# Performance work log

Measured on AMD Instinct MI355X. Metric: run time of the kernel, lower is better.

## Reference

```python
import jax, jax.numpy as jnp
import numpy as np

B, T, C, L = 1024, 1024, 96, 32
BLANK = C - 1          # tf.compat.v1.nn.ctc_loss uses num_classes-1 as blank
S = 2 * L + 1          # extended label length (blanks interleaved)
NEG = -1e30            # log-space 'zero'


def setup_inputs() -> dict:
    key = jax.random.key(0)
    k1, k2 = jax.random.split(key)
    y_true = jax.random.randint(k1, (B, L), 0, BLANK).astype(jnp.int64)  # labels in [0, C-2]
    y_pred = jax.random.normal(k2, (B, T, C), dtype=jnp.float32)          # pre-softmax logits
    return {"y_true": y_true, "y_pred": y_pred}


def _ctc_loss(y_pred, y_true):
    # y_pred: [B,T,C] logits, y_true: [B,L] int labels. All lengths are full
    # (label_length = L, input_length = T), matching the layer's call().
    logp = jax.nn.log_softmax(y_pred, axis=-1)                   # [B,T,C]
    # extended labels: blank, l0, blank, l1, ..., blank  -> [B,S]
    ext = jnp.full((B, S), BLANK, dtype=jnp.int32).at[:, 1::2].set(y_true.astype(jnp.int32))
    # skip transition allowed where ext[s] != blank and ext[s] != ext[s-2]
    skip = jnp.concatenate(
        [jnp.zeros((B, 2), bool), (ext[:, 2:] != BLANK) & (ext[:, 2:] != ext[:, :-2])],
        axis=1)                                                  # [B,S]
    # per-time emission log-probs of extended labels: [T,B,S]
    lp_ext = jnp.take_along_axis(logp, ext[:, None, :], axis=2)  # [B,T,S]
    lp_ext = jnp.transpose(lp_ext, (1, 0, 2))                    # [T,B,S]

    alpha0 = (jnp.full((B, S), NEG, dtype=logp.dtype)
              .at[:, 0].set(lp_ext[0, :, 0])
              .at[:, 1].set(lp_ext[0, :, 1]))

    def step(alpha, lp_t):
        a_stay = alpha
        a_prev = jnp.concatenate([jnp.full((B, 1), NEG, alpha.dtype), alpha[:, :-1]], axis=1)
        a_skip = jnp.concatenate([jnp.full((B, 2), NEG, alpha.dtype), alpha[:, :-2]], axis=1)
        a_skip = jnp.where(skip, a_skip, NEG)
        m = jnp.maximum(jnp.maximum(a_stay, a_prev), a_skip)
        new = m + jnp.log(jnp.exp(a_stay - m) + jnp.exp(a_prev - m) + jnp.exp(a_skip - m))
        return new + lp_t, None

    alphaT, _ = jax.lax.scan(step, alpha0, lp_ext[1:])
    # total log-likelihood ends at last blank or last label
    end = jnp.stack([alphaT[:, S - 1], alphaT[:, S - 2]], axis=0)  # [2,B]
    loss = -jax.scipy.special.logsumexp(end, axis=0)               # [B]
    return loss[:, None]                                           # [B,1], as ctc_batch_cost


def reference(y_true, y_pred):
    return _ctc_loss(y_pred, y_true)
```

## Files before the change

kernel.cpp:

```cpp
#include <hip/hip_runtime.h>


#define NB 1024
#define NT 1024
#define NC 96
#define NL 32
#define NEGF (-1e30f)
#define CHUNK 32
#define NCHUNK (NT / CHUNK)
#define SLOTF 97
#define LOG2E 1.4426950408889634f
#define LN2   0.69314718055994531f

__device__ __forceinline__ float fexp2(float x) { return __builtin_amdgcn_exp2f(x); }
__device__ __forceinline__ float flog2(float x) { return __builtin_amdgcn_logf(x); }

template <int CTRL>
__device__ __forceinline__ float dpp_mov(float v) {
  return __int_as_float(__builtin_amdgcn_update_dpp(
      __float_as_int(v), __float_as_int(v), CTRL, 0xF, 0xF, false));
}
__device__ __forceinline__ float dpp_shr1(float oldv, float v) {
  return __int_as_float(__builtin_amdgcn_update_dpp(
      __float_as_int(oldv), __float_as_int(v), 0x138, 0xF, 0xF, false));
}

__global__ __launch_bounds__(256) void ctc_fused(const int* __restrict__ yt,
                                                 const float* __restrict__ yp,
                                                 float* __restrict__ out) {
  __shared__ float ring[2 * CHUNK * SLOTF];

  const int b = blockIdx.x;
  const int wid = threadIdx.x >> 6;
  const int lane = threadIdx.x & 63;

  const float* __restrict__ xrow = yp + (size_t)b * NT * NC;

  const int cw = b & 3;
  const bool is_cons = (wid == cw);
  const int pr = ((wid - cw + 4) & 3) - 1;

  int extc = 95;
  bool skipf = false;
  if (is_cons) {
    const int* lab = yt + b * NL;
    if ((lane & 1) == 0) {
      const int j = lane >> 1;
      extc = lab[j];
      skipf = (j > 0) && (extc != lab[j - 1]);
    }
    __builtin_amdgcn_s_setprio(1);
  }

  const int rsel = lane >> 5;
  const int l32 = lane & 31;

  float UA[6][3], UB[6][3];

  auto load_regs = [&](float (&U)[6][3], int t0) {
    const float* rp = xrow + (size_t)(t0 + 2 * pr + rsel) * NC + l32;
#pragma unroll
    for (int jj = 0; jj < 6; ++jj) {
      if (pr + 3 * jj < 16) {
        U[jj][0] = rp[jj * 6 * NC + 0];
        U[jj][1] = rp[jj * 6 * NC + 32];
        U[jj][2] = rp[jj * 6 * NC + 64];
      }
    }
  };

  auto compute_store = [&](float (&U)[6][3], int cc) {
    float* wb = ring + (cc & 1) * (CHUNK * SLOTF) + (2 * pr + rsel) * SLOTF + l32;
#pragma unroll
    for (int jj = 0; jj < 6; ++jj) {
      if (pr + 3 * jj < 16) {
        const float u0 = U[jj][0] * LOG2E;
        const float u1 = U[jj][1] * LOG2E;
        const float u2 = U[jj][2] * LOG2E;
        float z = fexp2(u0) + fexp2(u1) + fexp2(u2);
        z += dpp_mov<0xB1>(z);
        z += dpp_mov<0x4E>(z);
        z += dpp_mov<0x124>(z);
        z += dpp_mov<0x128>(z);
        z += __shfl_xor(z, 16);
        const float lz = flog2(z);
        wb[jj * 6 * SLOTF + 0]  = u0 - lz;
        wb[jj * 6 * SLOTF + 32] = u1 - lz;
        wb[jj * 6 * SLOTF + 64] = u2 - lz;
      }
    }
  };

  float alpha = NEGF;
  float a0 = NEGF;

  auto consume = [&](int cc, bool first) {
    const float* hb = ring + (cc & 1) * (CHUNK * SLOTF) + extc;
    const float* hb95 = ring + (cc & 1) * (CHUNK * SLOTF) + 95;
    float lq[4], lqb[4];
    lq[0] = hb[0 * SLOTF];  lqb[0] = hb95[0 * SLOTF];
    lq[1] = hb[1 * SLOTF];  lqb[1] = hb95[1 * SLOTF];
    lq[2] = hb[2 * SLOTF];  lqb[2] = hb95[2 * SLOTF];
    lq[3] = 0.0f;           lqb[3] = 0.0f;
#pragma unroll
    for (int tt = 0; tt < CHUNK; ++tt) {
      const float lp = lq[tt & 3];
      const float lpb = lqb[tt & 3];
      if (tt + 3 < CHUNK) {
        lq[(tt + 3) & 3] = hb[(tt + 3) * SLOTF];
        lqb[(tt + 3) & 3] = hb95[(tt + 3) * SLOTF];
      }
      if (first && tt == 0) {
        a0 = lpb;
        alpha = (lane == 0) ? lp : NEGF;
      } else {
        const float ap = dpp_shr1(a0, alpha);
        float as = dpp_shr1(NEGF, ap);
        as = skipf ? as : NEGF;
        float mm, mid, mn;
        asm("v_max3_f32 %0, %1, %2, %3" : "=v"(mm) : "v"(alpha), "v"(ap), "v"(as));
        asm("v_med3_f32 %0, %1, %2, %3" : "=v"(mid) : "v"(alpha), "v"(ap), "v"(as));
        asm("v_min3_f32 %0, %1, %2, %3" : "=v"(mn) : "v"(alpha), "v"(ap), "v"(as));
        const float sm = (1.0f + fexp2(mid - mm)) + fexp2(mn - mm);
        alpha = (mm + lp) + flog2(sm);
        a0 += lpb;
      }
    }
  };

  if (!is_cons) load_regs(UA, 0);

  for (int c = 0; c < NCHUNK; c += 2) {
    if (!is_cons) {
      if (c + 1 < NCHUNK) load_regs(UB, (c + 1) * CHUNK);
      compute_store(UA, c);
      __syncthreads();
      if (c + 2 < NCHUNK) load_regs(UA, (c + 2) * CHUNK);
      compute_store(UB, c + 1);
      __syncthreads();
    } else {
      __syncthreads();
      if (c == 0) consume(0, true);
      else consume(c, false);
      __syncthreads();
      consume(c + 1, false);
    }
  }

  if (is_cons) {
    const float aS1 = __shfl(alpha, 63);
    const float aS2 = __shfl(alpha, 62);
    if (lane == 0) {
      const float mF = fmaxf(aS1, aS2);
      const float r = mF + flog2(fexp2(aS1 - mF) + fexp2(aS2 - mF));
      out[b] = -r * LN2;
    }
  }
}

extern "C" void kernel_launch(void* const* d_in, const int* in_sizes, int n_in,
                              void* d_out, int out_size, void* d_ws, size_t ws_size,
                              hipStream_t stream) {
  const int* yt = (const int*)d_in[0];
  const float* yp = (const float*)d_in[1];
  float* out = (float*)d_out;
  hipLaunchKernelGGL(ctc_fused, dim3(NB), dim3(256), 0, stream, yt, yp, out);
}
```

Baseline: 86.50 us.

## Process two batch elements per block with interleaved alpha recursions

Each block now handles two batch elements, so the consumer wave runs two independent CTC alpha recursions interleaved in one loop and the producer waves compute log-softmax rows for both. The grid is halved to 512 blocks. The aim is to hide the serial dependency latency of the DPP/exp/log recursion through instruction-level parallelism across the two chains. In exchange, producer register use doubles (four 18-float buffers), LDS per block doubles, and there are fewer blocks to spread across CUs.

```diff
diff --git a/kernel.cpp b/kernel.cpp
--- a/kernel.cpp
+++ b/kernel.cpp
@@ -2,6 +2,7 @@
 
 
 #define NB 1024
+#define NBLK 512
 #define NT 1024
 #define NC 96
 #define NL 32
@@ -9,6 +10,7 @@
 #define CHUNK 32
 #define NCHUNK (NT / CHUNK)
 #define SLOTF 97
+#define RINGF (2 * CHUNK * SLOTF)
 #define LOG2E 1.4426950408889634f
 #define LN2   0.69314718055994531f
 
@@ -28,26 +30,31 @@
 __global__ __launch_bounds__(256) void ctc_fused(const int* __restrict__ yt,
                                                  const float* __restrict__ yp,
                                                  float* __restrict__ out) {
-  __shared__ float ring[2 * CHUNK * SLOTF];
+  __shared__ float ring[2][RINGF];
 
   const int b = blockIdx.x;
   const int wid = threadIdx.x >> 6;
   const int lane = threadIdx.x & 63;
 
-  const float* __restrict__ xrow = yp + (size_t)b * NT * NC;
+  const int e0 = 2 * b, e1 = 2 * b + 1;
+  const float* __restrict__ xrow0 = yp + (size_t)e0 * NT * NC;
+  const float* __restrict__ xrow1 = yp + (size_t)e1 * NT * NC;
 
   const int cw = b & 3;
   const bool is_cons = (wid == cw);
   const int pr = ((wid - cw + 4) & 3) - 1;
 
-  int extc = 95;
-  bool skipf = false;
+  int ext0 = 95, ext1 = 95;
+  bool skip0 = false, skip1 = false;
   if (is_cons) {
-    const int* lab = yt + b * NL;
+    const int* lab0 = yt + e0 * NL;
+    const int* lab1 = yt + e1 * NL;
     if ((lane & 1) == 0) {
       const int j = lane >> 1;
-      extc = lab[j];
-      skipf = (j > 0) && (extc != lab[j - 1]);
+      ext0 = lab0[j];
+      skip0 = (j > 0) && (ext0 != lab0[j - 1]);
+      ext1 = lab1[j];
+      skip1 = (j > 0) && (ext1 != lab1[j - 1]);
     }
     __builtin_amdgcn_s_setprio(1);
   }
@@ -55,10 +62,10 @@
   const int rsel = lane >> 5;
   const int l32 = lane & 31;
 
-  float UA[6][3], UB[6][3];
-
-  auto load_regs = [&](float (&U)[6][3], int t0) {
-    const float* rp = xrow + (size_t)(t0 + 2 * pr + rsel) * NC + l32;
+  float UA0[6][3], UA1[6][3], UB0[6][3], UB1[6][3];
+
+  auto load_one = [&](float (&U)[6][3], const float* xr, int t0) {
+    const float* rp = xr + (size_t)(t0 + 2 * pr + rsel) * NC + l32;
 #pragma unroll
     for (int jj = 0; jj < 6; ++jj) {
       if (pr + 3 * jj < 16) {
@@ -69,8 +76,8 @@
     }
   };
 
-  auto compute_store = [&](float (&U)[6][3], int cc) {
-    float* wb = ring + (cc & 1) * (CHUNK * SLOTF) + (2 * pr + rsel) * SLOTF + l32;
+  auto store_one = [&](float (&U)[6][3], float* rg, int cc) {
+    float* wb = rg + (cc & 1) * (CHUNK * SLOTF) + (2 * pr + rsel) * SLOTF + l32;
 #pragma unroll
     for (int jj = 0; jj < 6; ++jj) {
       if (pr + 3 * jj < 16) {
@@ -91,52 +98,89 @@
     }
   };
 
-  float alpha = NEGF;
-  float a0 = NEGF;
+  float alpha0 = NEGF, alpha1 = NEGF;
+  float a00 = NEGF, a01 = NEGF;
+
+  auto step0 = [&](float lp, float lpb) {
+    const float ap = dpp_shr1(a00, alpha0);
+    float as = dpp_shr1(NEGF, ap);
+    as = skip0 ? as : NEGF;
+    float mm, mid, mn;
+    asm("v_max3_f32 %0, %1, %2, %3" : "=v"(mm) : "v"(alpha0), "v"(ap), "v"(as));
+    asm("v_med3_f32 %0, %1, %2, %3" : "=v"(mid) : "v"(alpha0), "v"(ap), "v"(as));
+    asm("v_min3_f32 %0, %1, %2, %3" : "=v"(mn) : "v"(alpha0), "v"(ap), "v"(as));
+    const float sm = (1.0f + fexp2(mid - mm)) + fexp2(mn - mm);
+    alpha0 = (mm + lp) + flog2(sm);
+    a00 += lpb;
+  };
+  auto step1 = [&](float lp, float lpb) {
+    const float ap = dpp_shr1(a01, alpha1);
+    float as = dpp_shr1(NEGF, ap);
+    as = skip1 ? as : NEGF;
+    float mm, mid, mn;
+    asm("v_max3_f32 %0, %1, %2, %3" : "=v"(mm) : "v"(alpha1), "v"(ap), "v"(as));
+    asm("v_med3_f32 %0, %1, %2, %3" : "=v"(mid) : "v"(alpha1), "v"(ap), "v"(as));
+    asm("v_min3_f32 %0, %1, %2, %3" : "=v"(mn) : "v"(alpha1), "v"(ap), "v"(as));
+    const float sm = (1.0f + fexp2(mid - mm)) + fexp2(mn - mm);
+    alpha1 = (mm + lp) + flog2(sm);
+    a01 += lpb;
+  };
 
   auto consume = [&](int cc, bool first) {
-    const float* hb = ring + (cc & 1) * (CHUNK * SLOTF) + extc;
-    const float* hb95 = ring + (cc & 1) * (CHUNK * SLOTF) + 95;
-    float lq[4], lqb[4];
-    lq[0] = hb[0 * SLOTF];  lqb[0] = hb95[0 * SLOTF];
-    lq[1] = hb[1 * SLOTF];  lqb[1] = hb95[1 * SLOTF];
-    lq[2] = hb[2 * SLOTF];  lqb[2] = hb95[2 * SLOTF];
-    lq[3] = 0.0f;           lqb[3] = 0.0f;
+    const float* h0 = ring[0] + (cc & 1) * (CHUNK * SLOTF) + ext0;
+    const float* h0b = ring[0] + (cc & 1) * (CHUNK * SLOTF) + 95;
+    const float* h1 = ring[1] + (cc & 1) * (CHUNK * SLOTF) + ext1;
+    const float* h1b = ring[1] + (cc & 1) * (CHUNK * SLOTF) + 95;
+    float q0[4], q0b[4], q1[4], q1b[4];
+#pragma unroll
+    for (int i = 0; i < 3; ++i) {
+      q0[i] = h0[i * SLOTF];
+      q0b[i] = h0b[i * SLOTF];
+      q1[i] = h1[i * SLOTF];
+      q1b[i] = h1b[i * SLOTF];
+    }
 #pragma unroll
     for (int tt = 0; tt < CHUNK; ++tt) {
-      const float lp = lq[tt & 3];
-      const float lpb = lqb[tt & 3];
+      const float lp0 = q0[tt & 3], lpb0 = q0b[tt & 3];
+      const float lp1 = q1[tt & 3], lpb1 = q1b[tt & 3];
       if (tt + 3 < CHUNK) {
-        lq[(tt + 3) & 3] = hb[(tt + 3) * SLOTF];
-        lqb[(tt + 3) & 3] = hb95[(tt + 3) * SLOTF];
+        q0[(tt + 3) & 3] = h0[(tt + 3) * SLOTF];
+        q0b[(tt + 3) & 3] = h0b[(tt + 3) * SLOTF];
+        q1[(tt + 3) & 3] = h1[(tt + 3) * SLOTF];
+        q1b[(tt + 3) & 3] = h1b[(tt + 3) * SLOTF];
       }
       if (first && tt == 0) {
-        a0 = lpb;
-        alpha = (lane == 0) ? lp : NEGF;
+        a00 = lpb0;
+        alpha0 = (lane == 0) ? lp0 : NEGF;
+        a01 = lpb1;
+        alpha1 = (lane == 0) ? lp1 : NEGF;
       } else {
-        const float ap = dpp_shr1(a0, alpha);
-        float as = dpp_shr1(NEGF, ap);
-        as = skipf ? as : NEGF;
-        float mm, mid, mn;
-        asm("v_max3_f32 %0, %1, %2, %3" : "=v"(mm) : "v"(alpha), "v"(ap), "v"(as));
-        asm("v_med3_f32 %0, %1, %2, %3" : "=v"(mid) : "v"(alpha), "v"(ap), "v"(as));
-        asm("v_min3_f32 %0, %1, %2, %3" : "=v"(mn) : "v"(alpha), "v"(ap), "v"(as));
-        const float sm = (1.0f + fexp2(mid - mm)) + fexp2(mn - mm);
-        alpha = (mm + lp) + flog2(sm);
-        a0 += lpb;
-      }
-    }
-  };
-
-  if (!is_cons) load_regs(UA, 0);
+        step0(lp0, lpb0);
+        step1(lp1, lpb1);
+      }
+    }
+  };
+
+  if (!is_cons) {
+    load_one(UA0, xrow0, 0);
+    load_one(UA1, xrow1, 0);
+  }
 
   for (int c = 0; c < NCHUNK; c += 2) {
     if (!is_cons) {
-      if (c + 1 < NCHUNK) load_regs(UB, (c + 1) * CHUNK);
-      compute_store(UA, c);
-      __syncthreads();
-      if (c + 2 < NCHUNK) load_regs(UA, (c + 2) * CHUNK);
-      compute_store(UB, c + 1);
+      if (c + 1 < NCHUNK) {
+        load_one(UB0, xrow0, (c + 1) * CHUNK);
+        load_one(UB1, xrow1, (c + 1) * CHUNK);
+      }
+      store_one(UA0, ring[0], c);
+      store_one(UA1, ring[1], c);
+      __syncthreads();
+      if (c + 2 < NCHUNK) {
+        load_one(UA0, xrow0, (c + 2) * CHUNK);
+        load_one(UA1, xrow1, (c + 2) * CHUNK);
+      }
+      store_one(UB0, ring[0], c + 1);
+      store_one(UB1, ring[1], c + 1);
       __syncthreads();
     } else {
       __syncthreads();
@@ -148,12 +192,15 @@
   }
 
   if (is_cons) {
-    const float aS1 = __shfl(alpha, 63);
-    const float aS2 = __shfl(alpha, 62);
+    const float a1_0 = __shfl(alpha0, 63);
+    const float a2_0 = __shfl(alpha0, 62);
+    const float a1_1 = __shfl(alpha1, 63);
+    const float a2_1 = __shfl(alpha1, 62);
     if (lane == 0) {
-      const float mF = fmaxf(aS1, aS2);
-      const float r = mF + flog2(fexp2(aS1 - mF) + fexp2(aS2 - mF));
-      out[b] = -r * LN2;
+      const float m0 = fmaxf(a1_0, a2_0);
+      out[e0] = -(m0 + flog2(fexp2(a1_0 - m0) + fexp2(a2_0 - m0))) * LN2;
+      const float m1 = fmaxf(a1_1, a2_1);
+      out[e1] = -(m1 + flog2(fexp2(a1_1 - m1) + fexp2(a2_1 - m1))) * LN2;
     }
   }
 }
@@ -164,5 +211,5 @@
   const int* yt = (const int*)d_in[0];
   const float* yp = (const float*)d_in[1];
   float* out = (float*)d_out;
-  hipLaunchKernelGGL(ctc_fused, dim3(NB), dim3(256), 0, stream, yt, yp, out);
-}
+  hipLaunchKernelGGL(ctc_fused, dim3(NBLK), dim3(256), 0, stream, yt, yp, out);
+}
```

Result: slower. 114.6 us (+32.5%).

## Process two batch elements per block with one producer wave per consumer

Applied to the files above, without the earlier changes.

Each block now handles two batch elements. Two waves run the serial alpha recursion and two waves act as producers, one per element, each computing the full 32-row log-softmax chunk into its own double-buffered LDS ring. This halves the grid and puts two latency-bound recursions in each block instead of one. In exchange each producer wave does twice the work per chunk, holds 96 floats per buffer in registers, and LDS use doubles, which may lower occupancy or make producers the bottleneck.

```diff
diff --git a/kernel.cpp b/kernel.cpp
--- a/kernel.cpp
+++ b/kernel.cpp
@@ -2,6 +2,7 @@
 
 
 #define NB 1024
+#define NBLK 512
 #define NT 1024
 #define NC 96
 #define NL 32
@@ -9,6 +10,7 @@
 #define CHUNK 32
 #define NCHUNK (NT / CHUNK)
 #define SLOTF 97
+#define RINGF (2 * CHUNK * SLOTF)
 #define LOG2E 1.4426950408889634f
 #define LN2   0.69314718055994531f
 
@@ -28,22 +30,24 @@
 __global__ __launch_bounds__(256) void ctc_fused(const int* __restrict__ yt,
                                                  const float* __restrict__ yp,
                                                  float* __restrict__ out) {
-  __shared__ float ring[2 * CHUNK * SLOTF];
+  __shared__ float ring[2][RINGF];
 
   const int b = blockIdx.x;
   const int wid = threadIdx.x >> 6;
   const int lane = threadIdx.x & 63;
 
-  const float* __restrict__ xrow = yp + (size_t)b * NT * NC;
+  const int cw = b & 3;
+  const int role = (wid - cw + 4) & 3;
+  const bool is_cons = (role < 2);
+  const int elem = 2 * b + (role & 1);
 
-  const int cw = b & 3;
-  const bool is_cons = (wid == cw);
-  const int pr = ((wid - cw + 4) & 3) - 1;
+  const float* __restrict__ xrow = yp + (size_t)elem * NT * NC;
+  float* rg = ring[role & 1];
 
   int extc = 95;
   bool skipf = false;
   if (is_cons) {
-    const int* lab = yt + b * NL;
+    const int* lab = yt + elem * NL;
     if ((lane & 1) == 0) {
       const int j = lane >> 1;
       extc = lab[j];
@@ -55,48 +59,59 @@
   const int rsel = lane >> 5;
   const int l32 = lane & 31;
 
-  float UA[6][3], UB[6][3];
+  float UA[16][3], UB[16][3];
 
-  auto load_regs = [&](float (&U)[6][3], int t0) {
-    const float* rp = xrow + (size_t)(t0 + 2 * pr + rsel) * NC + l32;
+  auto load_regs = [&](float (&U)[16][3], int t0) {
+    const float* rp = xrow + (size_t)(t0 + rsel) * NC + l32;
 #pragma unroll
-    for (int jj = 0; jj < 6; ++jj) {
-      if (pr + 3 * jj < 16) {
-        U[jj][0] = rp[jj * 6 * NC + 0];
-        U[jj][1] = rp[jj * 6 * NC + 32];
-        U[jj][2] = rp[jj * 6 * NC + 64];
-      }
+    for (int p = 0; p < 16; ++p) {
+      const float* q = rp + (size_t)(2 * p) * NC;
+      U[p][0] = q[0];
+      U[p][1] = q[32];
+      U[p][2] = q[64];
     }
   };
 
-  auto compute_store = [&](float (&U)[6][3], int cc) {
-    float* wb = ring + (cc & 1) * (CHUNK * SLOTF) + (2 * pr + rsel) * SLOTF + l32;
+  auto compute_store = [&](float (&U)[16][3], int cc) {
+    float* wb = rg + (cc & 1) * (CHUNK * SLOTF) + rsel * SLOTF + l32;
 #pragma unroll
-    for (int jj = 0; jj < 6; ++jj) {
-      if (pr + 3 * jj < 16) {
-        const float u0 = U[jj][0] * LOG2E;
-        const float u1 = U[jj][1] * LOG2E;
-        const float u2 = U[jj][2] * LOG2E;
-        float z = fexp2(u0) + fexp2(u1) + fexp2(u2);
-        z += dpp_mov<0xB1>(z);
-        z += dpp_mov<0x4E>(z);
-        z += dpp_mov<0x124>(z);
-        z += dpp_mov<0x128>(z);
-        z += __shfl_xor(z, 16);
-        const float lz = flog2(z);
-        wb[jj * 6 * SLOTF + 0]  = u0 - lz;
-        wb[jj * 6 * SLOTF + 32] = u1 - lz;
-        wb[jj * 6 * SLOTF + 64] = u2 - lz;
-      }
+    for (int p = 0; p < 16; ++p) {
+      const float u0 = U[p][0] * LOG2E;
+      const float u1 = U[p][1] * LOG2E;
+      const float u2 = U[p][2] * LOG2E;
+      float z = fexp2(u0) + fexp2(u1) + fexp2(u2);
+      z += dpp_mov<0xB1>(z);
+      z += dpp_mov<0x4E>(z);
+      z += dpp_mov<0x124>(z);
+      z += dpp_mov<0x128>(z);
+      z += __shfl_xor(z, 16);
+      const float lz = flog2(z);
+      float* w = wb + 2 * p * SLOTF;
+      w[0]  = u0 - lz;
+      w[32] = u1 - lz;
+      w[64] = u2 - lz;
     }
   };
 
   float alpha = NEGF;
   float a0 = NEGF;
 
+  auto lse_step = [&](float lp, float lpb) {
+    const float ap = dpp_shr1(a0, alpha);
+    float as = dpp_shr1(NEGF, ap);
+    as = skipf ? as : NEGF;
+    float mm, mid, mn;
+    asm("v_max3_f32 %0, %1, %2, %3" : "=v"(mm) : "v"(alpha), "v"(ap), "v"(as));
+    asm("v_med3_f32 %0, %1, %2, %3" : "=v"(mid) : "v"(alpha), "v"(ap), "v"(as));
+    asm("v_min3_f32 %0, %1, %2, %3" : "=v"(mn) : "v"(alpha), "v"(ap), "v"(as));
+    const float sm = (1.0f + fexp2(mid - mm)) + fexp2(mn - mm);
+    alpha = (mm + lp) + flog2(sm);
+    a0 += lpb;
+  };
+
   auto consume = [&](int cc, bool first) {
-    const float* hb = ring + (cc & 1) * (CHUNK * SLOTF) + extc;
-    const float* hb95 = ring + (cc & 1) * (CHUNK * SLOTF) + 95;
+    const float* hb = rg + (cc & 1) * (CHUNK * SLOTF) + extc;
+    const float* hb95 = rg + (cc & 1) * (CHUNK * SLOTF) + 95;
     float lq[4], lqb[4];
     lq[0] = hb[0 * SLOTF];  lqb[0] = hb95[0 * SLOTF];
     lq[1] = hb[1 * SLOTF];  lqb[1] = hb95[1 * SLOTF];
@@ -114,16 +129,7 @@
         a0 = lpb;
         alpha = (lane == 0) ? lp : NEGF;
       } else {
-        const float ap = dpp_shr1(a0, alpha);
-        float as = dpp_shr1(NEGF, ap);
-        as = skipf ? as : NEGF;
-        float mm, mid, mn;
-        asm("v_max3_f32 %0, %1, %2, %3" : "=v"(mm) : "v"(alpha), "v"(ap), "v"(as));
-        asm("v_med3_f32 %0, %1, %2, %3" : "=v"(mid) : "v"(alpha), "v"(ap), "v"(as));
-        asm("v_min3_f32 %0, %1, %2, %3" : "=v"(mn) : "v"(alpha), "v"(ap), "v"(as));
-        const float sm = (1.0f + fexp2(mid - mm)) + fexp2(mn - mm);
-        alpha = (mm + lp) + flog2(sm);
-        a0 += lpb;
+        lse_step(lp, lpb);
       }
     }
   };
@@ -153,7 +159,7 @@
     if (lane == 0) {
       const float mF = fmaxf(aS1, aS2);
       const float r = mF + flog2(fexp2(aS1 - mF) + fexp2(aS2 - mF));
-      out[b] = -r * LN2;
+      out[elem] = -r * LN2;
     }
   }
 }
@@ -164,5 +170,5 @@
   const int* yt = (const int*)d_in[0];
   const float* yp = (const float*)d_in[1];
   float* out = (float*)d_out;
-  hipLaunchKernelGGL(ctc_fused, dim3(NB), dim3(256), 0, stream, yt, yp, out);
+  hipLaunchKernelGGL(ctc_fused, dim3(NBLK), dim3(256), 0, stream, yt, yp, out);
 }
```

After: 93.87 us. 8.5% more time.
